# Kernel optimization log

Hardware: AMD Instinct MI355X
Metric: run time of the kernel (lower is better)

The kernel has to match this reference:

```python
import jax, jax.numpy as jnp
import numpy as np

N_NODES = 100000
N_EDGES = 1600000
D = 128
L = 3


def setup_inputs() -> dict:
    key = jax.random.key(0)
    k1, k2, k3 = jax.random.split(key, 3)
    edge_index = jax.random.randint(k1, (2, N_EDGES), 0, N_NODES, dtype=jnp.int64)
    emb = jax.random.normal(k2, (N_NODES, D), dtype=jnp.float32)
    # Glorot-style scale for the per-layer linear weights
    Ws = jax.random.normal(k3, (L, D, D), dtype=jnp.float32) * (1.0 / np.sqrt(D))
    bs = jnp.zeros((L, D), dtype=jnp.float32)
    return {"edge_index": edge_index, "emb": emb, "Ws": Ws, "bs": bs}


def _gcn_forward(emb, Ws, bs, edge_index):
    n = emb.shape[0]
    self_loop = jnp.arange(n, dtype=edge_index.dtype)
    # PyG GCNConv adds self-loops and uses symmetric normalization
    row = jnp.concatenate([edge_index[0], self_loop])  # source nodes
    col = jnp.concatenate([edge_index[1], self_loop])  # target nodes
    deg = jax.ops.segment_sum(jnp.ones(row.shape[0], dtype=emb.dtype), col, num_segments=n)
    deg_inv_sqrt = jnp.where(deg > 0, jax.lax.rsqrt(jnp.maximum(deg, 1.0)), 0.0)
    norm = deg_inv_sqrt[row] * deg_inv_sqrt[col]  # [E+N]

    x = emb
    for l in range(Ws.shape[0]):
        h = x @ Ws[l]                              # [N, D] linear transform
        msg = h[row] * norm[:, None]               # gather + scale [E+N, D]
        x = jax.ops.segment_sum(msg, col, num_segments=n) + bs[l]  # scatter-add
        x = jax.nn.relu(x)                         # dropout is identity in eval
    return x


def reference(edge_index, emb, Ws, bs) -> jnp.ndarray:
    return _gcn_forward(emb, Ws, bs, edge_index)
```

## Files before the change

### kernel.cpp

```cpp
#include <hip/hip_runtime.h>
#include <hip/hip_fp16.h>
#include <cstdint>
#include <cstddef>

#define N_NODES 100000
#define N_EDGES 1600000
#define D 128
#define NLAYERS 3
#define NB 3125
#define NBLK_E 128
#define EPB 12500
#define ENT_CAP 1024

typedef float f2v __attribute__((ext_vector_type(2)));
typedef float f4v __attribute__((ext_vector_type(4)));
typedef _Float16 f16x8 __attribute__((ext_vector_type(8)));
typedef float f32x4 __attribute__((ext_vector_type(4)));
typedef unsigned u32x4 __attribute__((ext_vector_type(4)));


__global__ __launch_bounds__(512) void hist1_kernel(const int* __restrict__ col,
                                                    int* __restrict__ hmat) {
    __shared__ int hist[NB];
    int b = blockIdx.x, t = threadIdx.x;
    for (int j = t; j < NB; j += 512) hist[j] = 0;
    __syncthreads();
    int base = b * EPB;
    for (int i = t; i < EPB; i += 512) {
        int c = col[base + i];
        atomicAdd(&hist[c >> 5], 1);
    }
    __syncthreads();
    for (int j = t; j < NB; j += 512) hmat[b * NB + j] = hist[j];
}

__global__ void btot_kernel(const int* __restrict__ hmat, int* __restrict__ btot) {
    int j = blockIdx.x * 256 + threadIdx.x;
    if (j < NB) {
        int s = 0;
        for (int b = 0; b < NBLK_E; b++) s += hmat[b * NB + j];
        btot[j] = s;
    }
}

__global__ void bscan_kernel(const int* __restrict__ btot, int* __restrict__ bstart, int nb, int e) {
    __shared__ int lsum[1024];
    int t = threadIdx.x;
    int vals[4];
    int v0 = 0;
#pragma unroll
    for (int j = 0; j < 4; j++) {
        int idx = t * 4 + j;
        int c = (idx < nb) ? btot[idx] : 0;
        vals[j] = c;
        v0 += c;
    }
    lsum[t] = v0;
    __syncthreads();
    for (int off = 1; off < 1024; off <<= 1) {
        int x = (t >= off) ? lsum[t - off] : 0;
        __syncthreads();
        lsum[t] += x;
        __syncthreads();
    }
    int base = lsum[t] - v0;
#pragma unroll
    for (int j = 0; j < 4; j++) {
        int idx = t * 4 + j;
        if (idx < nb) {
            bstart[idx] = base;
            base += vals[j];
        }
    }
    if (t == 0) bstart[nb] = e;
}

__global__ void hoff_kernel(const int* __restrict__ hmat, const int* __restrict__ bstart,
                            int* __restrict__ hoff) {
    int j = blockIdx.x * 256 + threadIdx.x;
    if (j < NB) {
        int run = bstart[j];
        for (int b = 0; b < NBLK_E; b++) {
            hoff[b * NB + j] = run;
            run += hmat[b * NB + j];
        }
    }
}

__global__ __launch_bounds__(512) void scatter_kernel(const int* __restrict__ row,
                                                      const int* __restrict__ col,
                                                      const int* __restrict__ hoff,
                                                      unsigned* __restrict__ bucketbuf) {
    __shared__ int cur[NB];
    int b = blockIdx.x, t = threadIdx.x;
    for (int j = t; j < NB; j += 512) cur[j] = hoff[b * NB + j];
    __syncthreads();
    int base = b * EPB;
    for (int i = t; i < EPB; i += 512) {
        int r = row[base + i], c = col[base + i];
        int pos = atomicAdd(&cur[c >> 5], 1);
        bucketbuf[pos] = ((unsigned)r << 5) | (unsigned)(c & 31);
    }
}

__global__ void fill2_kernel(const unsigned* __restrict__ bucketbuf, const int* __restrict__ bstart,
                             int* __restrict__ offsets, float* __restrict__ dinv,
                             int* __restrict__ src, int n, int e) {
    __shared__ unsigned ent[ENT_CAP];
    __shared__ int hist[32];
    __shared__ int cur[32];
    __shared__ int loff[32];
    int b = blockIdx.x, t = threadIdx.x;
    int s0 = bstart[b];
    int cnt = bstart[b + 1] - s0;
    if (cnt > ENT_CAP) cnt = ENT_CAP;
    if (t < 32) hist[t] = 0;
    __syncthreads();
    for (int i = t; i < cnt; i += 256) {
        unsigned v = bucketbuf[s0 + i];
        ent[i] = v;
        atomicAdd(&hist[v & 31], 1);
    }
    __syncthreads();
    if (t == 0) {
        int run = s0;
#pragma unroll
        for (int j = 0; j < 32; j++) {
            loff[j] = run;
            run += hist[j];
        }
    }
    __syncthreads();
    if (t < 32) {
        int node = b * 32 + t;
        int o = loff[t];
        offsets[node] = o;
        cur[t] = o;
        dinv[node] = rsqrtf((float)(hist[t] + 1));
    }
    if (b == 0 && t == 0) offsets[n] = e;
    __syncthreads();
    for (int i = t; i < cnt; i += 256) {
        unsigned v = ent[i];
        int pos = atomicAdd(&cur[v & 31], 1);
        src[pos] = (int)(v >> 5);
    }
}


__global__ void cast_kernel(const float2* __restrict__ in, const float* __restrict__ dinv,
                            __half2* __restrict__ out, int n2) {
    int i = blockIdx.x * 256 + threadIdx.x;
    if (i < n2) {
        float d = dinv[i >> 6];
        float2 v = in[i];
        out[i] = __floats2half2_rn(d * v.x, d * v.y);
    }
}

__global__ void wsplit_kernel(const float* __restrict__ W,
                              _Float16* __restrict__ Wh, _Float16* __restrict__ Wl) {
    int c = blockIdx.x, l = blockIdx.y, k = threadIdx.x;
    float w = W[(size_t)l * 16384 + k * 128 + c];
    _Float16 h = (_Float16)w;
    float r = w - (float)h;
    Wh[(size_t)l * 16384 + c * 128 + k] = h;
    Wl[(size_t)l * 16384 + c * 128 + k] = (_Float16)r;
}

__global__ void agg_kernel(const __half2* __restrict__ xs, const int* __restrict__ offs,
                           unsigned* __restrict__ Ah, unsigned* __restrict__ Al,
                           const float* __restrict__ dinv, const int* __restrict__ src) {
    int v = blockIdx.x;
    int f = threadIdx.x;
    float dv = dinv[v];
    float2 a0 = __half22float2(xs[(size_t)v * 64 + f]);
    float ax = a0.x;
    float ay = a0.y;
    int i = offs[v], s1 = offs[v + 1];
    for (; i + 7 < s1; i += 8) {
        int s[8];
#pragma unroll
        for (int j = 0; j < 8; j++) s[j] = src[i + j];
        float2 x[8];
#pragma unroll
        for (int j = 0; j < 8; j++) x[j] = __half22float2(xs[(size_t)s[j] * 64 + f]);
#pragma unroll
        for (int j = 0; j < 8; j++) {
            ax += x[j].x;
            ay += x[j].y;
        }
    }
    if (i < s1) {
        int last = s1 - 1;
        int s[8];
        float m[8];
#pragma unroll
        for (int j = 0; j < 8; j++) {
            int idx = i + j;
            bool in = idx < s1;
            s[j] = src[in ? idx : last];
            m[j] = in ? 1.0f : 0.0f;
        }
        float2 x[8];
#pragma unroll
        for (int j = 0; j < 8; j++) x[j] = __half22float2(xs[(size_t)s[j] * 64 + f]);
#pragma unroll
        for (int j = 0; j < 8; j++) {
            ax += m[j] * x[j].x;
            ay += m[j] * x[j].y;
        }
    }
    float rx = dv * ax, ry = dv * ay;
    __half2 h2 = __floats2half2_rn(rx, ry);
    float2 hb = __half22float2(h2);
    __half2 l2 = __floats2half2_rn(rx - hb.x, ry - hb.y);
    __builtin_nontemporal_store(__builtin_bit_cast(unsigned, h2), Ah + (size_t)v * 64 + f);
    __builtin_nontemporal_store(__builtin_bit_cast(unsigned, l2), Al + (size_t)v * 64 + f);
}

__global__ __launch_bounds__(256, 6) void gemm_mfma_kernel(
    const _Float16* __restrict__ Ahp, const _Float16* __restrict__ Alp,
    const _Float16* __restrict__ Whp, const _Float16* __restrict__ Wlp,
    const float* __restrict__ bias, float* __restrict__ out,
    __half2* __restrict__ xs_out, const float* __restrict__ dinv,
    int write_h, int write_out) {
    __shared__ _Float16 sA[2][32][136];
    int t = threadIdx.x;
    int f = t & 63;
    int w = t >> 6;
    int row0 = blockIdx.x * 32;

    const u32x4* Aq[2] = {(const u32x4*)Ahp, (const u32x4*)Alp};
#pragma unroll
    for (int i = 0; i < 4; i++) {
        int qid = t + 256 * i;
        int p = qid >> 9;
        int rem = qid & 511;
        int r = rem >> 4;
        int k2 = rem & 15;
        u32x4 v = __builtin_nontemporal_load(&Aq[p][(size_t)(row0 + r) * 16 + k2]);
        *(u32x4*)&sA[p][r][k2 * 8] = v;
    }
    __syncthreads();

    int lrow = f & 15, kg = f >> 4;
    f32x4 acc[2][2];
#pragma unroll
    for (int m = 0; m < 2; m++)
#pragma unroll
        for (int c = 0; c < 2; c++) acc[m][c] = (f32x4){0.f, 0.f, 0.f, 0.f};

#pragma unroll
    for (int ks = 0; ks < 4; ks++) {
        int g = ks * 4 + kg;
        f16x8 a0h = *(const f16x8*)&sA[0][lrow][g * 8];
        f16x8 a0l = *(const f16x8*)&sA[1][lrow][g * 8];
        f16x8 a1h = *(const f16x8*)&sA[0][16 + lrow][g * 8];
        f16x8 a1l = *(const f16x8*)&sA[1][16 + lrow][g * 8];
#pragma unroll
        for (int c = 0; c < 2; c++) {
            int col = w * 32 + c * 16 + lrow;
            f16x8 bh = *(const f16x8*)&Whp[(size_t)col * 128 + g * 8];
            f16x8 bl = *(const f16x8*)&Wlp[(size_t)col * 128 + g * 8];
            acc[0][c] = __builtin_amdgcn_mfma_f32_16x16x32_f16(a0h, bh, acc[0][c], 0, 0, 0);
            acc[0][c] = __builtin_amdgcn_mfma_f32_16x16x32_f16(a0l, bh, acc[0][c], 0, 0, 0);
            acc[0][c] = __builtin_amdgcn_mfma_f32_16x16x32_f16(a0h, bl, acc[0][c], 0, 0, 0);
            acc[1][c] = __builtin_amdgcn_mfma_f32_16x16x32_f16(a1h, bh, acc[1][c], 0, 0, 0);
            acc[1][c] = __builtin_amdgcn_mfma_f32_16x16x32_f16(a1l, bh, acc[1][c], 0, 0, 0);
            acc[1][c] = __builtin_amdgcn_mfma_f32_16x16x32_f16(a1h, bl, acc[1][c], 0, 0, 0);
        }
    }

    float bcol[2];
    bcol[0] = bias[w * 32 + 0 * 16 + lrow];
    bcol[1] = bias[w * 32 + 1 * 16 + lrow];
#pragma unroll
    for (int m = 0; m < 2; m++) {
        int rbase = row0 + m * 16 + kg * 4;
#pragma unroll
        for (int j = 0; j < 4; j++) {
            int rowi = rbase + j;
            float dvr = write_h ? dinv[rowi] : 0.f;
#pragma unroll
            for (int c = 0; c < 2; c++) {
                float o = fmaxf(acc[m][c][j] + bcol[c], 0.f);
                float o2 = __shfl_xor(o, 1);
                int col = w * 32 + c * 16 + lrow;
                if (write_out)
                    __builtin_nontemporal_store(o, out + (size_t)rowi * 128 + col);
                if (write_h && !(f & 1))
                    xs_out[(size_t)rowi * 64 + (col >> 1)] =
                        __floats2half2_rn(dvr * o, dvr * o2);
            }
        }
    }
}


extern "C" void kernel_launch(void* const* d_in, const int* in_sizes, int n_in,
                              void* d_out, int out_size, void* d_ws, size_t ws_size,
                              hipStream_t stream) {
    const int* edge = (const int*)d_in[0];
    const float* emb = (const float*)d_in[1];
    const float* Ws = (const float*)d_in[2];
    const float* bs = (const float*)d_in[3];
    float* out = (float*)d_out;

    const int n = N_NODES, e = N_EDGES;
    const int* row = edge;
    const int* col = edge + e;

    char* p = (char*)d_ws;
    _Float16* Ah = (_Float16*)p;
    int* hmat = (int*)p;
    int* hoff = hmat + (size_t)NBLK_E * NB;
    p += (size_t)n * D * 2;
    _Float16* Al = (_Float16*)p;
    p += (size_t)n * D * 2;
    __half2* xs = (__half2*)p;
    unsigned* bucketbuf = (unsigned*)p;
    p += (size_t)n * D * 2;
    int* csr_src  = (int*)p;    p += (size_t)e * 4;
    float* dinv   = (float*)p;  p += (size_t)n * 4;
    int* offsets  = (int*)p;    p += (size_t)(n + 1) * 4;
    int* btot     = (int*)p;    p += (size_t)NB * 4;
    int* bstart   = (int*)p;    p += (size_t)(NB + 1) * 4;
    _Float16* WhT = (_Float16*)p; p += (size_t)NLAYERS * D * D * 2;
    _Float16* WlT = (_Float16*)p; p += (size_t)NLAYERS * D * D * 2;

    hist1_kernel<<<NBLK_E, 512, 0, stream>>>(col, hmat);
    btot_kernel<<<(NB + 255) / 256, 256, 0, stream>>>(hmat, btot);
    bscan_kernel<<<1, 1024, 0, stream>>>(btot, bstart, NB, e);
    hoff_kernel<<<(NB + 255) / 256, 256, 0, stream>>>(hmat, bstart, hoff);
    scatter_kernel<<<NBLK_E, 512, 0, stream>>>(row, col, hoff, bucketbuf);
    fill2_kernel<<<NB, 256, 0, stream>>>(bucketbuf, bstart, offsets, dinv, csr_src, n, e);
    wsplit_kernel<<<dim3(128, NLAYERS), 128, 0, stream>>>(Ws, WhT, WlT);

    int n2 = n * 64;
    cast_kernel<<<(n2 + 255) / 256, 256, 0, stream>>>((const float2*)emb, dinv, xs, n2);

    for (int l = 0; l < NLAYERS; l++) {
        agg_kernel<<<n, 64, 0, stream>>>(xs, offsets, (unsigned*)Ah, (unsigned*)Al,
                                         dinv, csr_src);
        gemm_mfma_kernel<<<n / 32, 256, 0, stream>>>(
            Ah, Al, WhT + (size_t)l * D * D, WlT + (size_t)l * D * D,
            bs + (size_t)l * D, out, xs, dinv,
            (l < NLAYERS - 1) ? 1 : 0, (l == NLAYERS - 1) ? 1 : 0);
    }
}
```

Before: 499.5 us.

## Replace bucketed CSR build with global atomics, widen gather unroll, split aggregation

```diff
diff --git a/kernel.cpp b/kernel.cpp
--- a/kernel.cpp
+++ b/kernel.cpp
@@ -7,144 +7,79 @@
 #define N_EDGES 1600000
 #define D 128
 #define NLAYERS 3
-#define NB 3125
-#define NBLK_E 128
-#define EPB 12500
-#define ENT_CAP 1024
+#define NSCAN 391
 
 typedef float f2v __attribute__((ext_vector_type(2)));
-typedef float f4v __attribute__((ext_vector_type(4)));
 typedef _Float16 f16x8 __attribute__((ext_vector_type(8)));
 typedef float f32x4 __attribute__((ext_vector_type(4)));
 typedef unsigned u32x4 __attribute__((ext_vector_type(4)));
 
 
-__global__ __launch_bounds__(512) void hist1_kernel(const int* __restrict__ col,
-                                                    int* __restrict__ hmat) {
-    __shared__ int hist[NB];
+__global__ void zero_kernel(int* __restrict__ deg, int n) {
+    int i = blockIdx.x * 256 + threadIdx.x;
+    if (i < n) deg[i] = 0;
+}
+
+__global__ void deg_kernel(const int* __restrict__ col, int* __restrict__ deg) {
+    int i = blockIdx.x * 256 + threadIdx.x;
+    atomicAdd(&deg[col[i]], 1);
+}
+
+__global__ __launch_bounds__(256) void scan1_kernel(const int* __restrict__ deg,
+                                                    int* __restrict__ offsets,
+                                                    int* __restrict__ totals, int n) {
+    __shared__ int lsum[256];
     int b = blockIdx.x, t = threadIdx.x;
-    for (int j = t; j < NB; j += 512) hist[j] = 0;
+    int idx = b * 256 + t;
+    int d = (idx < n) ? deg[idx] : 0;
+    lsum[t] = d;
     __syncthreads();
-    int base = b * EPB;
-    for (int i = t; i < EPB; i += 512) {
-        int c = col[base + i];
-        atomicAdd(&hist[c >> 5], 1);
-    }
-    __syncthreads();
-    for (int j = t; j < NB; j += 512) hmat[b * NB + j] = hist[j];
-}
-
-__global__ void btot_kernel(const int* __restrict__ hmat, int* __restrict__ btot) {
-    int j = blockIdx.x * 256 + threadIdx.x;
-    if (j < NB) {
-        int s = 0;
-        for (int b = 0; b < NBLK_E; b++) s += hmat[b * NB + j];
-        btot[j] = s;
-    }
-}
-
-__global__ void bscan_kernel(const int* __restrict__ btot, int* __restrict__ bstart, int nb, int e) {
-    __shared__ int lsum[1024];
-    int t = threadIdx.x;
-    int vals[4];
-    int v0 = 0;
-#pragma unroll
-    for (int j = 0; j < 4; j++) {
-        int idx = t * 4 + j;
-        int c = (idx < nb) ? btot[idx] : 0;
-        vals[j] = c;
-        v0 += c;
-    }
-    lsum[t] = v0;
-    __syncthreads();
-    for (int off = 1; off < 1024; off <<= 1) {
+    for (int off = 1; off < 256; off <<= 1) {
         int x = (t >= off) ? lsum[t - off] : 0;
         __syncthreads();
         lsum[t] += x;
         __syncthreads();
     }
-    int base = lsum[t] - v0;
-#pragma unroll
-    for (int j = 0; j < 4; j++) {
-        int idx = t * 4 + j;
-        if (idx < nb) {
-            bstart[idx] = base;
-            base += vals[j];
-        }
-    }
-    if (t == 0) bstart[nb] = e;
-}
-
-__global__ void hoff_kernel(const int* __restrict__ hmat, const int* __restrict__ bstart,
-                            int* __restrict__ hoff) {
-    int j = blockIdx.x * 256 + threadIdx.x;
-    if (j < NB) {
-        int run = bstart[j];
-        for (int b = 0; b < NBLK_E; b++) {
-            hoff[b * NB + j] = run;
-            run += hmat[b * NB + j];
-        }
-    }
-}
-
-__global__ __launch_bounds__(512) void scatter_kernel(const int* __restrict__ row,
-                                                      const int* __restrict__ col,
-                                                      const int* __restrict__ hoff,
-                                                      unsigned* __restrict__ bucketbuf) {
-    __shared__ int cur[NB];
+    if (idx < n) offsets[idx] = lsum[t] - d;
+    if (t == 255) totals[b] = lsum[255];
+}
+
+__global__ __launch_bounds__(512) void scan2_kernel(int* __restrict__ totals, int nb) {
+    __shared__ int lsum[512];
+    int t = threadIdx.x;
+    int d = (t < nb) ? totals[t] : 0;
+    lsum[t] = d;
+    __syncthreads();
+    for (int off = 1; off < 512; off <<= 1) {
+        int x = (t >= off) ? lsum[t - off] : 0;
+        __syncthreads();
+        lsum[t] += x;
+        __syncthreads();
+    }
+    if (t < nb) totals[t] = lsum[t] - d;
+}
+
+__global__ __launch_bounds__(256) void scan3_kernel(const int* __restrict__ deg,
+                                                    int* __restrict__ offsets,
+                                                    const int* __restrict__ totals,
+                                                    int* __restrict__ cur,
+                                                    float* __restrict__ dinv, int n, int e) {
     int b = blockIdx.x, t = threadIdx.x;
-    for (int j = t; j < NB; j += 512) cur[j] = hoff[b * NB + j];
-    __syncthreads();
-    int base = b * EPB;
-    for (int i = t; i < EPB; i += 512) {
-        int r = row[base + i], c = col[base + i];
-        int pos = atomicAdd(&cur[c >> 5], 1);
-        bucketbuf[pos] = ((unsigned)r << 5) | (unsigned)(c & 31);
-    }
-}
-
-__global__ void fill2_kernel(const unsigned* __restrict__ bucketbuf, const int* __restrict__ bstart,
-                             int* __restrict__ offsets, float* __restrict__ dinv,
-                             int* __restrict__ src, int n, int e) {
-    __shared__ unsigned ent[ENT_CAP];
-    __shared__ int hist[32];
-    __shared__ int cur[32];
-    __shared__ int loff[32];
-    int b = blockIdx.x, t = threadIdx.x;
-    int s0 = bstart[b];
-    int cnt = bstart[b + 1] - s0;
-    if (cnt > ENT_CAP) cnt = ENT_CAP;
-    if (t < 32) hist[t] = 0;
-    __syncthreads();
-    for (int i = t; i < cnt; i += 256) {
-        unsigned v = bucketbuf[s0 + i];
-        ent[i] = v;
-        atomicAdd(&hist[v & 31], 1);
-    }
-    __syncthreads();
-    if (t == 0) {
-        int run = s0;
-#pragma unroll
-        for (int j = 0; j < 32; j++) {
-            loff[j] = run;
-            run += hist[j];
-        }
-    }
-    __syncthreads();
-    if (t < 32) {
-        int node = b * 32 + t;
-        int o = loff[t];
-        offsets[node] = o;
-        cur[t] = o;
-        dinv[node] = rsqrtf((float)(hist[t] + 1));
+    int idx = b * 256 + t;
+    if (idx < n) {
+        int off = offsets[idx] + totals[b];
+        offsets[idx] = off;
+        cur[idx] = off;
+        dinv[idx] = rsqrtf((float)(deg[idx] + 1));
     }
     if (b == 0 && t == 0) offsets[n] = e;
-    __syncthreads();
-    for (int i = t; i < cnt; i += 256) {
-        unsigned v = ent[i];
-        int pos = atomicAdd(&cur[v & 31], 1);
-        src[pos] = (int)(v >> 5);
-    }
+}
+
+__global__ void scatter2_kernel(const int* __restrict__ row, const int* __restrict__ col,
+                                int* __restrict__ cur, int* __restrict__ src) {
+    int i = blockIdx.x * 256 + threadIdx.x;
+    int pos = atomicAdd(&cur[col[i]], 1);
+    src[pos] = row[i];
 }
 
 
@@ -170,15 +105,29 @@
 
 __global__ void agg_kernel(const __half2* __restrict__ xs, const int* __restrict__ offs,
                            unsigned* __restrict__ Ah, unsigned* __restrict__ Al,
-                           const float* __restrict__ dinv, const int* __restrict__ src) {
-    int v = blockIdx.x;
+                           const float* __restrict__ dinv, const int* __restrict__ src,
+                           int vbase) {
+    int v = vbase + blockIdx.x;
     int f = threadIdx.x;
     float dv = dinv[v];
     float2 a0 = __half22float2(xs[(size_t)v * 64 + f]);
     float ax = a0.x;
     float ay = a0.y;
     int i = offs[v], s1 = offs[v + 1];
-    for (; i + 7 < s1; i += 8) {
+    for (; i + 15 < s1; i += 16) {
+        int s[16];
+#pragma unroll
+        for (int j = 0; j < 16; j++) s[j] = src[i + j];
+        float2 x[16];
+#pragma unroll
+        for (int j = 0; j < 16; j++) x[j] = __half22float2(xs[(size_t)s[j] * 64 + f]);
+#pragma unroll
+        for (int j = 0; j < 16; j++) {
+            ax += x[j].x;
+            ay += x[j].y;
+        }
+    }
+    if (i + 7 < s1) {
         int s[8];
 #pragma unroll
         for (int j = 0; j < 8; j++) s[j] = src[i + j];
@@ -190,6 +139,7 @@
             ax += x[j].x;
             ay += x[j].y;
         }
+        i += 8;
     }
     if (i < s1) {
         int last = s1 - 1;
@@ -313,36 +263,37 @@
 
     char* p = (char*)d_ws;
     _Float16* Ah = (_Float16*)p;
-    int* hmat = (int*)p;
-    int* hoff = hmat + (size_t)NBLK_E * NB;
+    int* deg = (int*)p;
+    int* cur = deg + N_NODES;
+    int* totals = cur + N_NODES;
     p += (size_t)n * D * 2;
     _Float16* Al = (_Float16*)p;
     p += (size_t)n * D * 2;
     __half2* xs = (__half2*)p;
-    unsigned* bucketbuf = (unsigned*)p;
     p += (size_t)n * D * 2;
     int* csr_src  = (int*)p;    p += (size_t)e * 4;
     float* dinv   = (float*)p;  p += (size_t)n * 4;
     int* offsets  = (int*)p;    p += (size_t)(n + 1) * 4;
-    int* btot     = (int*)p;    p += (size_t)NB * 4;
-    int* bstart   = (int*)p;    p += (size_t)(NB + 1) * 4;
     _Float16* WhT = (_Float16*)p; p += (size_t)NLAYERS * D * D * 2;
     _Float16* WlT = (_Float16*)p; p += (size_t)NLAYERS * D * D * 2;
 
-    hist1_kernel<<<NBLK_E, 512, 0, stream>>>(col, hmat);
-    btot_kernel<<<(NB + 255) / 256, 256, 0, stream>>>(hmat, btot);
-    bscan_kernel<<<1, 1024, 0, stream>>>(btot, bstart, NB, e);
-    hoff_kernel<<<(NB + 255) / 256, 256, 0, stream>>>(hmat, bstart, hoff);
-    scatter_kernel<<<NBLK_E, 512, 0, stream>>>(row, col, hoff, bucketbuf);
-    fill2_kernel<<<NB, 256, 0, stream>>>(bucketbuf, bstart, offsets, dinv, csr_src, n, e);
+    zero_kernel<<<NSCAN, 256, 0, stream>>>(deg, n);
+    deg_kernel<<<e / 256, 256, 0, stream>>>(col, deg);
+    scan1_kernel<<<NSCAN, 256, 0, stream>>>(deg, offsets, totals, n);
+    scan2_kernel<<<1, 512, 0, stream>>>(totals, NSCAN);
+    scan3_kernel<<<NSCAN, 256, 0, stream>>>(deg, offsets, totals, cur, dinv, n, e);
+    scatter2_kernel<<<e / 256, 256, 0, stream>>>(row, col, cur, csr_src);
     wsplit_kernel<<<dim3(128, NLAYERS), 128, 0, stream>>>(Ws, WhT, WlT);
 
     int n2 = n * 64;
     cast_kernel<<<(n2 + 255) / 256, 256, 0, stream>>>((const float2*)emb, dinv, xs, n2);
 
+    const int half = n / 2;
     for (int l = 0; l < NLAYERS; l++) {
-        agg_kernel<<<n, 64, 0, stream>>>(xs, offsets, (unsigned*)Ah, (unsigned*)Al,
-                                         dinv, csr_src);
+        agg_kernel<<<half, 64, 0, stream>>>(xs, offsets, (unsigned*)Ah, (unsigned*)Al,
+                                            dinv, csr_src, 0);
+        agg_kernel<<<half, 64, 0, stream>>>(xs, offsets, (unsigned*)Ah, (unsigned*)Al,
+                                            dinv, csr_src, half);
         gemm_mfma_kernel<<<n / 32, 256, 0, stream>>>(
             Ah, Al, WhT + (size_t)l * D * D, WlT + (size_t)l * D * D,
             bs + (size_t)l * D, out, xs, dinv,
```

Measured after the change: 626.5 us. +25.4%, slower.
